# Optimization experiments

Hardware: AMD Instinct MI355X
Metric: run time of the kernel (lower is better)

## Reference

```python
import jax, jax.numpy as jnp
import numpy as np

IN_FEATURES = 4096
OUT_FEATURES = 4096
K = 0.5  # keep top-k fraction of weights by |score|


def setup_inputs() -> dict:
    key = jax.random.key(0)
    kx, kw, ks = jax.random.split(key, 3)
    x = jax.random.normal(kx, (8192, IN_FEATURES), dtype=jnp.float32)
    # kaiming_normal_(mode='fan_in', nonlinearity='relu'): std = sqrt(2/fan_in)
    std = float(np.sqrt(2.0 / IN_FEATURES))
    weights = jax.random.normal(kw, (OUT_FEATURES, IN_FEATURES), dtype=jnp.float32) * std
    bias = jnp.zeros((OUT_FEATURES,), dtype=jnp.float32)
    # scores init to ones in torch, but perturb so the top-k selection is non-degenerate
    scores = jnp.ones((OUT_FEATURES, IN_FEATURES), dtype=jnp.float32) + 0.01 * jax.random.normal(ks, (OUT_FEATURES, IN_FEATURES), dtype=jnp.float32)
    return {"x": x, "weights": weights, "bias": bias, "scores": scores}


def _topk_mask(s):
    # Reproduces torch sort-based thresholding: flatten, sort ascending,
    # bottom j = int((1-K)*n) entries -> 0, remaining top entries -> 1.
    flat = s.ravel()
    n = flat.shape[0]
    j = int((1.0 - K) * n)
    order = jnp.argsort(flat)  # ascending
    keep = (jnp.arange(n) >= j).astype(s.dtype)
    mask_flat = jnp.zeros((n,), dtype=s.dtype).at[order].set(keep)
    return mask_flat.reshape(s.shape)


def reference(x, weights, bias, scores):
    s = jnp.abs(scores)
    hard = _topk_mask(s)
    # straight-through estimator: forward uses hard mask, grad passes to |scores|
    mask = s + jax.lax.stop_gradient(hard - s)
    pruned = weights * mask  # [out, in]
    return x @ pruned.T + bias  # [B, out]
```

## Files before the change

### kernel.cpp

```cpp
#include <hip/hip_runtime.h>


#define NTOT   16777216u
#define JDROP  8388608u
#define MDIM   8192
#define NDIM   4096
#define KDIM   4096

typedef __bf16 v8bf __attribute__((ext_vector_type(8)));
typedef float  v4f  __attribute__((ext_vector_type(4)));

__device__ __forceinline__ unsigned short f2bf(float f){
  unsigned u = __float_as_uint(f);
  u += 0x7fffu + ((u >> 16) & 1u);
  return (unsigned short)(u >> 16);
}

__global__ void zero_hist(unsigned* hist, unsigned* h15g){
  h15g[blockIdx.x*256 + threadIdx.x] = 0u;
  if (blockIdx.x==0) hist[threadIdx.x] = 0u;
}

__global__ __launch_bounds__(256) void hist_pass(const float* __restrict__ scores,
                                                 unsigned* __restrict__ hist,
                                                 const unsigned* __restrict__ state,
                                                 int p){
  __shared__ __align__(16) unsigned char pc[256*256];
  int tid = threadIdx.x;
  unsigned* pz = (unsigned*)pc;
  #pragma unroll
  for (int k=0;k<64;++k) pz[tid + k*256] = 0u;
  __syncthreads();
  unsigned prefix = (p>0) ? state[0] : 0u;
  const float4* s4 = (const float4*)(scores + (size_t)blockIdx.x * 16384);
  for (int it=0; it<16; ++it){
    float4 v = s4[(size_t)it*256 + tid];
    #pragma unroll
    for (int e=0;e<4;++e){
      float f = (e==0)?v.x:(e==1)?v.y:(e==2)?v.z:v.w;
      unsigned u = __float_as_uint(f) & 0x7fffffffu;
      unsigned d, ok;
      if (p==0){ d = u>>23;         ok = 1u; }
      else     { d = (u>>15)&0xffu; ok = ((u>>23)==prefix); }
      if (ok) pc[d*256 + tid]++;
    }
  }
  __syncthreads();
  unsigned b = (unsigned)tid;
  const unsigned* row = (const unsigned*)(pc + b*256);
  unsigned s = 0;
  for (int kk=0;kk<64;++kk){
    int k = (kk + tid) & 63;
    unsigned w = row[k];
    s += (w & 0xffu) + ((w>>8)&0xffu) + ((w>>16)&0xffu) + (w>>24);
  }
  if (s) atomicAdd(&hist[b], s);
}

__global__ void select_pass(unsigned* hist, unsigned* state, int p){
  int lane = threadIdx.x;
  unsigned c[4];
  #pragma unroll
  for (int k=0;k<4;++k){ c[k] = hist[lane*4+k]; hist[lane*4+k] = 0u; }
  unsigned s = c[0]+c[1]+c[2]+c[3];
  unsigned inc = s;
  #pragma unroll
  for (int d=1; d<64; d<<=1){
    unsigned t = (unsigned)__shfl_up((int)inc, d, 64);
    if (lane >= d) inc += t;
  }
  unsigned excl = inc - s;
  unsigned target = (p==0) ? JDROP : state[1];
  unsigned oldpre = (p==0) ? 0u    : state[0];
  if (target >= excl && target < excl + s){
    unsigned cum = excl, digit = 0, below = 0;
    #pragma unroll
    for (int k=0;k<4;++k){
      if (target < cum + c[k]){ digit = (unsigned)lane*4u + (unsigned)k; below = cum; break; }
      cum += c[k];
    }
    state[0] = (oldpre << 8) | digit;
    state[1] = target - below;
  }
}

__global__ __launch_bounds__(512) void hist15_pass(const float* __restrict__ scores,
                                                   const unsigned* __restrict__ state,
                                                   unsigned* __restrict__ h15g){
  __shared__ unsigned h[32768];
  int tid = threadIdx.x;
  #pragma unroll
  for (int k=0;k<64;++k) h[tid + k*512] = 0u;
  __syncthreads();
  const unsigned pre16 = state[0];
  const float4* s4 = (const float4*)scores;
  const size_t base = (size_t)blockIdx.x * 16384;
  for (int it=0; it<32; ++it){
    float4 v = s4[base + (size_t)it*512 + tid];
    #pragma unroll
    for (int e=0;e<4;++e){
      float f = (e==0)?v.x:(e==1)?v.y:(e==2)?v.z:v.w;
      unsigned u = __float_as_uint(f) & 0x7fffffffu;
      if ((u>>15) == pre16) atomicAdd(&h[u & 0x7fffu], 1u);
    }
  }
  __syncthreads();
  #pragma unroll
  for (int k=0;k<64;++k){
    unsigned v = h[tid + k*512];
    if (v) atomicAdd(&h15g[tid + k*512], v);
  }
}

__global__ __launch_bounds__(256) void select15(const unsigned* __restrict__ h15g,
                                                unsigned* state){
  int tid = threadIdx.x;
  unsigned s = 0;
  for (int k=0;k<128;++k) s += h15g[tid*128 + k];
  __shared__ unsigned sc[256];
  sc[tid] = s; __syncthreads();
  for (int d=1; d<256; d<<=1){
    unsigned t = (tid >= d) ? sc[tid-d] : 0u;
    __syncthreads();
    sc[tid] += t;
    __syncthreads();
  }
  unsigned excl = sc[tid] - s;
  unsigned target = state[1];
  if (target >= excl && target < excl + s){
    unsigned cum = excl, digit = 0, below = 0;
    for (int k=0;k<128;++k){
      unsigned c = h15g[tid*128 + k];
      if (target < cum + c){ digit = (unsigned)(tid*128 + k); below = cum; break; }
      cum += c;
    }
    state[0] = (state[0] << 15) | digit;
    state[1] = target - below;
  }
}

__global__ __launch_bounds__(256) void tie_count(const float* __restrict__ scores,
                                                 const unsigned* __restrict__ state,
                                                 unsigned* __restrict__ tieCnt){
  unsigned T = state[0];
  int tid = threadIdx.x;
  const float4* s4 = (const float4*)(scores + (size_t)blockIdx.x * 4096);
  unsigned cnt = 0;
  for (int it=0; it<4; ++it){
    float4 v = s4[it*256 + tid];
    #pragma unroll
    for (int e=0;e<4;++e){
      float f = (e==0)?v.x:(e==1)?v.y:(e==2)?v.z:v.w;
      unsigned u = __float_as_uint(f) & 0x7fffffffu;
      cnt += (u == T) ? 1u : 0u;
    }
  }
  __shared__ unsigned r[256];
  r[tid] = cnt; __syncthreads();
  for (int s=128; s>0; s>>=1){ if (tid < s) r[tid] += r[tid+s]; __syncthreads(); }
  if (tid==0) tieCnt[blockIdx.x] = r[0];
}

__global__ __launch_bounds__(256) void build_pruned(const float* __restrict__ scores,
                                                    const float* __restrict__ w,
                                                    const unsigned* __restrict__ state,
                                                    const unsigned* __restrict__ tieCnt,
                                                    unsigned short* __restrict__ wpr){
  const int tid  = threadIdx.x;
  const int lane = tid & 63;
  const int wv   = tid >> 6;
  const int rowFirst = blockIdx.x*4;
  const int row  = rowFirst + wv;

  unsigned part = 0;
  for (int j = tid; j < rowFirst; j += 256) part += tieCnt[j];
  __shared__ unsigned red[256];
  red[tid] = part; __syncthreads();
  for (int s=128; s>0; s>>=1){ if (tid < s) red[tid] += red[tid+s]; __syncthreads(); }
  unsigned runBase = red[0];
  #pragma unroll
  for (int i=0;i<3;++i) if (i < wv) runBase += tieCnt[rowFirst + i];

  const unsigned T = state[0], D = state[1];
  const float4* s4 = (const float4*)(scores + (size_t)row*4096);
  const float4* w4 = (const float4*)(w      + (size_t)row*4096);
  ushort4*      o4 = (ushort4*)(wpr + (size_t)row*4096);
  const unsigned long long below = (lane==0)?0ull:((~0ull) >> (64-lane));
  for (int it=0; it<16; ++it){
    float4 sv = s4[it*64 + lane];
    float4 wvv = w4[it*64 + lane];
    unsigned u0 = __float_as_uint(sv.x) & 0x7fffffffu;
    unsigned u1 = __float_as_uint(sv.y) & 0x7fffffffu;
    unsigned u2 = __float_as_uint(sv.z) & 0x7fffffffu;
    unsigned u3 = __float_as_uint(sv.w) & 0x7fffffffu;
    bool t0=(u0==T), t1=(u1==T), t2=(u2==T), t3=(u3==T);
    unsigned long long b0=__ballot(t0), b1=__ballot(t1), b2=__ballot(t2), b3=__ballot(t3);
    unsigned lanesBelow = (unsigned)(__popcll(b0&below)+__popcll(b1&below)
                                   + __popcll(b2&below)+__popcll(b3&below));
    unsigned base = runBase + lanesBelow;
    unsigned r0 = base;
    unsigned r1 = base + (t0?1u:0u);
    unsigned r2 = r1   + (t1?1u:0u);
    unsigned r3 = r2   + (t2?1u:0u);
    bool k0 = (u0>T) || (t0 && r0>=D);
    bool k1 = (u1>T) || (t1 && r1>=D);
    bool k2 = (u2>T) || (t2 && r2>=D);
    bool k3 = (u3>T) || (t3 && r3>=D);
    ushort4 o;
    o.x = k0 ? f2bf(wvv.x) : (unsigned short)0;
    o.y = k1 ? f2bf(wvv.y) : (unsigned short)0;
    o.z = k2 ? f2bf(wvv.z) : (unsigned short)0;
    o.w = k3 ? f2bf(wvv.w) : (unsigned short)0;
    o4[it*64 + lane] = o;
    runBase += (unsigned)(__popcll(b0)+__popcll(b1)+__popcll(b2)+__popcll(b3));
  }
}

__global__ __launch_bounds__(256) void convert_x(const float4* __restrict__ x,
                                                 ushort4* __restrict__ xb){
  size_t i = (size_t)blockIdx.x * 256 + threadIdx.x;
  float4 v = x[i];
  ushort4 o; o.x=f2bf(v.x); o.y=f2bf(v.y); o.z=f2bf(v.z); o.w=f2bf(v.w);
  xb[i] = o;
}

__device__ __forceinline__ void gload_lds16b(const void* g, void* l){
  __builtin_amdgcn_global_load_lds(
      (__attribute__((address_space(1))) void*)g,
      (__attribute__((address_space(3))) void*)l, 16, 0, 0);
}

__device__ __forceinline__ void stage_mat(const unsigned short* __restrict__ G, int rowBase,
                                          unsigned short (* __restrict__ S)[64],
                                          int kt, int wid, int lane){
  #pragma unroll
  for (int hj=0; hj<4; ++hj){
    const int rg0 = (hj>>1)*128 + (wid*2 + (hj&1))*8;
    const int rg  = rg0 + (lane>>3);
    const int c16 = (lane&7) ^ (rg & 7);
    gload_lds16b(G + (size_t)(rowBase + rg)*KDIM + kt*64 + c16*8, &S[rg0][0]);
  }
}

__device__ __forceinline__ v8bf ldsfrag(const unsigned short (* __restrict__ S)[64],
                                        int row, int kc){
  return *(const v8bf*)&S[row][(kc ^ (row & 7))*8];
}

#define BAR()   { __builtin_amdgcn_s_barrier(); asm volatile("" ::: "memory"); }
#define LGKM0() asm volatile("s_waitcnt lgkmcnt(0)" ::: "memory")

__device__ __forceinline__ void ktile(const unsigned short* __restrict__ A,
                                      const unsigned short* __restrict__ B,
                                      unsigned short (* __restrict__ Asq)[64],
                                      unsigned short (* __restrict__ Bsq)[64],
                                      int Mb, int Nb, int t,
                                      int wr, int wc, int wid, int lane,
                                      v4f acc[8][4]){
  const int r16 = lane & 15, kg = lane >> 4;
  const bool pf = (t + 2 < KDIM/64);

  v8bf a0[4][2], b0[2][2];
  #pragma unroll
  for (int i=0;i<4;++i)
    #pragma unroll
    for (int ks=0;ks<2;++ks)
      a0[i][ks] = ldsfrag(Asq, wr*128 + i*16 + r16, ks*4 + kg);
  #pragma unroll
  for (int n=0;n<2;++n)
    #pragma unroll
    for (int ks=0;ks<2;++ks)
      b0[n][ks] = ldsfrag(Bsq, wc*64 + n*16 + r16, ks*4 + kg);
  BAR(); LGKM0();
  __builtin_amdgcn_s_setprio(1);
  #pragma unroll
  for (int i=0;i<4;++i)
    #pragma unroll
    for (int n=0;n<2;++n)
      #pragma unroll
      for (int ks=0;ks<2;++ks)
        acc[i][n] = __builtin_amdgcn_mfma_f32_16x16x32_bf16(a0[i][ks], b0[n][ks], acc[i][n], 0,0,0);
  __builtin_amdgcn_s_setprio(0);
  BAR();

  v8bf b1[2][2];
  #pragma unroll
  for (int n=0;n<2;++n)
    #pragma unroll
    for (int ks=0;ks<2;++ks)
      b1[n][ks] = ldsfrag(Bsq, wc*64 + (2+n)*16 + r16, ks*4 + kg);
  BAR(); LGKM0();
  __builtin_amdgcn_s_setprio(1);
  #pragma unroll
  for (int i=0;i<4;++i)
    #pragma unroll
    for (int n=0;n<2;++n)
      #pragma unroll
      for (int ks=0;ks<2;++ks)
        acc[i][2+n] = __builtin_amdgcn_mfma_f32_16x16x32_bf16(a0[i][ks], b1[n][ks], acc[i][2+n], 0,0,0);
  __builtin_amdgcn_s_setprio(0);
  BAR();

  v8bf a1[4][2];
  #pragma unroll
  for (int i=0;i<4;++i)
    #pragma unroll
    for (int ks=0;ks<2;++ks)
      a1[i][ks] = ldsfrag(Asq, wr*128 + 64 + i*16 + r16, ks*4 + kg);
  if (pf) stage_mat(B, Nb, Bsq, t+2, wid, lane);
  BAR(); LGKM0();
  __builtin_amdgcn_s_setprio(1);
  #pragma unroll
  for (int i=0;i<4;++i)
    #pragma unroll
    for (int n=0;n<2;++n)
      #pragma unroll
      for (int ks=0;ks<2;++ks)
        acc[4+i][n] = __builtin_amdgcn_mfma_f32_16x16x32_bf16(a1[i][ks], b0[n][ks], acc[4+i][n], 0,0,0);
  __builtin_amdgcn_s_setprio(0);
  BAR();

  if (pf) stage_mat(A, Mb, Asq, t+2, wid, lane);
  __builtin_amdgcn_s_setprio(1);
  #pragma unroll
  for (int i=0;i<4;++i)
    #pragma unroll
    for (int n=0;n<2;++n)
      #pragma unroll
      for (int ks=0;ks<2;++ks)
        acc[4+i][2+n] = __builtin_amdgcn_mfma_f32_16x16x32_bf16(a1[i][ks], b1[n][ks], acc[4+i][2+n], 0,0,0);
  __builtin_amdgcn_s_setprio(0);
  if (pf) { asm volatile("s_waitcnt vmcnt(8)" ::: "memory"); }
  else    { asm volatile("s_waitcnt vmcnt(0)" ::: "memory"); }
  BAR();
}

__global__ __launch_bounds__(512, 2) void gemm256(const unsigned short* __restrict__ A,
                                                  const unsigned short* __restrict__ B,
                                                  const float* __restrict__ bias,
                                                  float* __restrict__ out){
  __shared__ __align__(16) unsigned short As[2][256][64];
  __shared__ __align__(16) unsigned short Bs[2][256][64];

  const int bid = blockIdx.x;
  const int swz = (bid & 7) * 64 + (bid >> 3);
  const int Mb  = (swz >> 4) * 256;
  const int Nb  = (swz & 15) * 256;

  const int tid  = threadIdx.x;
  const int lane = tid & 63;
  const int wid  = tid >> 6;
  const int wr   = wid >> 2;
  const int wc   = wid & 3;

  v4f acc[8][4];
  #pragma unroll
  for (int i=0;i<8;++i)
    #pragma unroll
    for (int n=0;n<4;++n) acc[i][n] = (v4f){0.f,0.f,0.f,0.f};

  stage_mat(A, Mb, As[0], 0, wid, lane);
  stage_mat(B, Nb, Bs[0], 0, wid, lane);
  stage_mat(A, Mb, As[1], 1, wid, lane);
  stage_mat(B, Nb, Bs[1], 1, wid, lane);
  asm volatile("s_waitcnt vmcnt(8)" ::: "memory");
  BAR();

  #pragma unroll 1
  for (int t = 0; t < KDIM/64; t += 2){
    ktile(A, B, As[0], Bs[0], Mb, Nb, t,   wr, wc, wid, lane, acc);
    ktile(A, B, As[1], Bs[1], Mb, Nb, t+1, wr, wc, wid, lane, acc);
  }

  #pragma unroll
  for (int mt=0; mt<8; ++mt){
    const int gm0 = Mb + wr*128 + mt*16 + (lane >> 4)*4;
    #pragma unroll
    for (int nt=0; nt<4; ++nt){
      const int gn = Nb + wc*64 + nt*16 + (lane & 15);
      const float bv = bias[gn];
      v4f a = acc[mt][nt];
      #pragma unroll
      for (int r=0; r<4; ++r)
        out[(size_t)(gm0 + r)*NDIM + gn] = a[r] + bv;
    }
  }
}

extern "C" void kernel_launch(void* const* d_in, const int* in_sizes, int n_in,
                              void* d_out, int out_size, void* d_ws, size_t ws_size,
                              hipStream_t stream){
  const float* x      = (const float*)d_in[0];
  const float* w      = (const float*)d_in[1];
  const float* bias   = (const float*)d_in[2];
  const float* scores = (const float*)d_in[3];
  float* out = (float*)d_out;

  char* ws = (char*)d_ws;
  unsigned* hist    = (unsigned*)(ws);
  unsigned* state   = (unsigned*)(ws + 1024);
  unsigned* tieCnt  = (unsigned*)(ws + 2048);
  unsigned short* xb  = (unsigned short*)(ws + 65536);
  unsigned short* wpr = (unsigned short*)(ws + 65536 + (size_t)MDIM*KDIM*2);
  unsigned* h15g = (unsigned*)(ws + 65536);

  zero_hist<<<128, 256, 0, stream>>>(hist, h15g);
  for (int p = 0; p < 2; ++p){
    hist_pass<<<1024, 256, 0, stream>>>(scores, hist, state, p);
    select_pass<<<1, 64, 0, stream>>>(hist, state, p);
  }
  hist15_pass<<<256, 512, 0, stream>>>(scores, state, h15g);
  select15<<<1, 256, 0, stream>>>(h15g, state);
  tie_count<<<4096, 256, 0, stream>>>(scores, state, tieCnt);
  build_pruned<<<1024, 256, 0, stream>>>(scores, w, state, tieCnt, wpr);
  convert_x<<<MDIM*KDIM/4/256, 256, 0, stream>>>((const float4*)x, (ushort4*)xb);

  gemm256<<<dim3(512), 512, 0, stream>>>(xb, wpr, bias, out);
}
```

Before: 682.0 us.

## Replace tie-count pass with atomic tie list and single-block fixup

The separate tie_count kernel, which re-read all scores to count threshold ties, is removed. build_pruned now keeps every element with |score| >= T and appends tied element indices to a global list via atomics. A small single-block kernel then zeroes the lowest-index ties needed to meet the exact drop count, using an O(n^2) rank over the ties. This saves a full read of the scores matrix plus the prefix reduction, but relies on the number of ties being small and capped. The explicit lgkmcnt(0) waits after barriers in the GEMM k-tile are also dropped, leaving LDS wait placement to the compiler.

```diff
diff --git a/kernel.cpp b/kernel.cpp
--- a/kernel.cpp
+++ b/kernel.cpp
@@ -6,6 +6,7 @@
 #define MDIM   8192
 #define NDIM   4096
 #define KDIM   4096
+#define TIECAP 1048576u
 
 typedef __bf16 v8bf __attribute__((ext_vector_type(8)));
 typedef float  v4f  __attribute__((ext_vector_type(4)));
@@ -16,9 +17,10 @@
   return (unsigned short)(u >> 16);
 }
 
-__global__ void zero_hist(unsigned* hist, unsigned* h15g){
+__global__ void zero_hist(unsigned* hist, unsigned* h15g, unsigned* tieCnt){
   h15g[blockIdx.x*256 + threadIdx.x] = 0u;
   if (blockIdx.x==0) hist[threadIdx.x] = 0u;
+  if (blockIdx.x==0 && threadIdx.x==0) *tieCnt = 0u;
 }
 
 __global__ __launch_bounds__(256) void hist_pass(const float* __restrict__ scores,
@@ -139,80 +141,52 @@
   }
 }
 
-__global__ __launch_bounds__(256) void tie_count(const float* __restrict__ scores,
-                                                 const unsigned* __restrict__ state,
-                                                 unsigned* __restrict__ tieCnt){
-  unsigned T = state[0];
-  int tid = threadIdx.x;
-  const float4* s4 = (const float4*)(scores + (size_t)blockIdx.x * 4096);
-  unsigned cnt = 0;
-  for (int it=0; it<4; ++it){
-    float4 v = s4[it*256 + tid];
-    #pragma unroll
-    for (int e=0;e<4;++e){
-      float f = (e==0)?v.x:(e==1)?v.y:(e==2)?v.z:v.w;
-      unsigned u = __float_as_uint(f) & 0x7fffffffu;
-      cnt += (u == T) ? 1u : 0u;
-    }
-  }
-  __shared__ unsigned r[256];
-  r[tid] = cnt; __syncthreads();
-  for (int s=128; s>0; s>>=1){ if (tid < s) r[tid] += r[tid+s]; __syncthreads(); }
-  if (tid==0) tieCnt[blockIdx.x] = r[0];
-}
-
 __global__ __launch_bounds__(256) void build_pruned(const float* __restrict__ scores,
                                                     const float* __restrict__ w,
                                                     const unsigned* __restrict__ state,
-                                                    const unsigned* __restrict__ tieCnt,
+                                                    unsigned* __restrict__ tieCnt,
+                                                    unsigned* __restrict__ tieList,
                                                     unsigned short* __restrict__ wpr){
-  const int tid  = threadIdx.x;
-  const int lane = tid & 63;
-  const int wv   = tid >> 6;
-  const int rowFirst = blockIdx.x*4;
-  const int row  = rowFirst + wv;
-
-  unsigned part = 0;
-  for (int j = tid; j < rowFirst; j += 256) part += tieCnt[j];
-  __shared__ unsigned red[256];
-  red[tid] = part; __syncthreads();
-  for (int s=128; s>0; s>>=1){ if (tid < s) red[tid] += red[tid+s]; __syncthreads(); }
-  unsigned runBase = red[0];
-  #pragma unroll
-  for (int i=0;i<3;++i) if (i < wv) runBase += tieCnt[rowFirst + i];
-
-  const unsigned T = state[0], D = state[1];
+  const int row  = blockIdx.x*4 + (threadIdx.x >> 6);
+  const int lane = threadIdx.x & 63;
+  const unsigned T = state[0];
   const float4* s4 = (const float4*)(scores + (size_t)row*4096);
   const float4* w4 = (const float4*)(w      + (size_t)row*4096);
   ushort4*      o4 = (ushort4*)(wpr + (size_t)row*4096);
-  const unsigned long long below = (lane==0)?0ull:((~0ull) >> (64-lane));
+  const unsigned rowBase = (unsigned)row * 4096u;
   for (int it=0; it<16; ++it){
     float4 sv = s4[it*64 + lane];
-    float4 wvv = w4[it*64 + lane];
+    float4 wv = w4[it*64 + lane];
     unsigned u0 = __float_as_uint(sv.x) & 0x7fffffffu;
     unsigned u1 = __float_as_uint(sv.y) & 0x7fffffffu;
     unsigned u2 = __float_as_uint(sv.z) & 0x7fffffffu;
     unsigned u3 = __float_as_uint(sv.w) & 0x7fffffffu;
-    bool t0=(u0==T), t1=(u1==T), t2=(u2==T), t3=(u3==T);
-    unsigned long long b0=__ballot(t0), b1=__ballot(t1), b2=__ballot(t2), b3=__ballot(t3);
-    unsigned lanesBelow = (unsigned)(__popcll(b0&below)+__popcll(b1&below)
-                                   + __popcll(b2&below)+__popcll(b3&below));
-    unsigned base = runBase + lanesBelow;
-    unsigned r0 = base;
-    unsigned r1 = base + (t0?1u:0u);
-    unsigned r2 = r1   + (t1?1u:0u);
-    unsigned r3 = r2   + (t2?1u:0u);
-    bool k0 = (u0>T) || (t0 && r0>=D);
-    bool k1 = (u1>T) || (t1 && r1>=D);
-    bool k2 = (u2>T) || (t2 && r2>=D);
-    bool k3 = (u3>T) || (t3 && r3>=D);
     ushort4 o;
-    o.x = k0 ? f2bf(wvv.x) : (unsigned short)0;
-    o.y = k1 ? f2bf(wvv.y) : (unsigned short)0;
-    o.z = k2 ? f2bf(wvv.z) : (unsigned short)0;
-    o.w = k3 ? f2bf(wvv.w) : (unsigned short)0;
+    o.x = (u0 >= T) ? f2bf(wv.x) : (unsigned short)0;
+    o.y = (u1 >= T) ? f2bf(wv.y) : (unsigned short)0;
+    o.z = (u2 >= T) ? f2bf(wv.z) : (unsigned short)0;
+    o.w = (u3 >= T) ? f2bf(wv.w) : (unsigned short)0;
     o4[it*64 + lane] = o;
-    runBase += (unsigned)(__popcll(b0)+__popcll(b1)+__popcll(b2)+__popcll(b3));
+    const unsigned ebase = rowBase + (unsigned)(it*64 + lane)*4u;
+    if (u0 == T){ unsigned p = atomicAdd(tieCnt,1u); if (p < TIECAP) tieList[p] = ebase;    }
+    if (u1 == T){ unsigned p = atomicAdd(tieCnt,1u); if (p < TIECAP) tieList[p] = ebase+1u; }
+    if (u2 == T){ unsigned p = atomicAdd(tieCnt,1u); if (p < TIECAP) tieList[p] = ebase+2u; }
+    if (u3 == T){ unsigned p = atomicAdd(tieCnt,1u); if (p < TIECAP) tieList[p] = ebase+3u; }
+  }
+}
+
+__global__ __launch_bounds__(256) void tie_fixup(const unsigned* __restrict__ tieCnt,
+                                                 const unsigned* __restrict__ tieList,
+                                                 const unsigned* __restrict__ state,
+                                                 unsigned short* __restrict__ wpr){
+  unsigned n = *tieCnt; if (n > TIECAP) n = TIECAP;
+  const unsigned D = state[1];
+  if (D == 0) return;
+  for (unsigned j = threadIdx.x; j < n; j += 256){
+    unsigned idx = tieList[j];
+    unsigned rank = 0;
+    for (unsigned k = 0; k < n; ++k) rank += (tieList[k] < idx) ? 1u : 0u;
+    if (rank < D) wpr[idx] = (unsigned short)0;
   }
 }
 
@@ -248,7 +222,6 @@
 }
 
 #define BAR()   { __builtin_amdgcn_s_barrier(); asm volatile("" ::: "memory"); }
-#define LGKM0() asm volatile("s_waitcnt lgkmcnt(0)" ::: "memory")
 
 __device__ __forceinline__ void ktile(const unsigned short* __restrict__ A,
                                       const unsigned short* __restrict__ B,
@@ -271,7 +244,7 @@
     #pragma unroll
     for (int ks=0;ks<2;++ks)
       b0[n][ks] = ldsfrag(Bsq, wc*64 + n*16 + r16, ks*4 + kg);
-  BAR(); LGKM0();
+  BAR();
   __builtin_amdgcn_s_setprio(1);
   #pragma unroll
   for (int i=0;i<4;++i)
@@ -289,7 +262,7 @@
     #pragma unroll
     for (int ks=0;ks<2;++ks)
       b1[n][ks] = ldsfrag(Bsq, wc*64 + (2+n)*16 + r16, ks*4 + kg);
-  BAR(); LGKM0();
+  BAR();
   __builtin_amdgcn_s_setprio(1);
   #pragma unroll
   for (int i=0;i<4;++i)
@@ -308,7 +281,7 @@
     for (int ks=0;ks<2;++ks)
       a1[i][ks] = ldsfrag(Asq, wr*128 + 64 + i*16 + r16, ks*4 + kg);
   if (pf) stage_mat(B, Nb, Bsq, t+2, wid, lane);
-  BAR(); LGKM0();
+  BAR();
   __builtin_amdgcn_s_setprio(1);
   #pragma unroll
   for (int i=0;i<4;++i)
@@ -402,17 +375,18 @@
   unsigned* tieCnt  = (unsigned*)(ws + 2048);
   unsigned short* xb  = (unsigned short*)(ws + 65536);
   unsigned short* wpr = (unsigned short*)(ws + 65536 + (size_t)MDIM*KDIM*2);
-  unsigned* h15g = (unsigned*)(ws + 65536);
-
-  zero_hist<<<128, 256, 0, stream>>>(hist, h15g);
+  unsigned* h15g    = (unsigned*)(ws + 65536);
+  unsigned* tieList = (unsigned*)(ws + 65536 + 33554432);
+
+  zero_hist<<<128, 256, 0, stream>>>(hist, h15g, tieCnt);
   for (int p = 0; p < 2; ++p){
     hist_pass<<<1024, 256, 0, stream>>>(scores, hist, state, p);
     select_pass<<<1, 64, 0, stream>>>(hist, state, p);
   }
   hist15_pass<<<256, 512, 0, stream>>>(scores, state, h15g);
   select15<<<1, 256, 0, stream>>>(h15g, state);
-  tie_count<<<4096, 256, 0, stream>>>(scores, state, tieCnt);
-  build_pruned<<<1024, 256, 0, stream>>>(scores, w, state, tieCnt, wpr);
+  build_pruned<<<1024, 256, 0, stream>>>(scores, w, state, tieCnt, tieList, wpr);
+  tie_fixup<<<1, 256, 0, stream>>>(tieCnt, tieList, state, wpr);
   convert_x<<<MDIM*KDIM/4/256, 256, 0, stream>>>((const float4*)x, (ushort4*)xb);
 
   gemm256<<<dim3(512), 512, 0, stream>>>(xb, wpr, bias, out);
```

Result: no change. 671.5 us (-1.5%).
